# Performance work log

Hardware: AMD Instinct MI355X
Metric: run time of the kernel (lower is better)

Reference implementation:

```python
import jax, jax.numpy as jnp
import numpy as np

B, S, L = 2048, 1024, 32
NEG = -10000.0


def setup_inputs() -> dict:
    key = jax.random.key(0)
    k1, k2, k3, k4 = jax.random.split(key, 4)
    lstm_scores = jax.random.normal(k1, (B, S, L), dtype=jnp.float32)
    word_seq_lens = jax.random.randint(k2, (B,), 1, S + 1)  # lengths in [1, S]
    tags = jax.random.randint(k3, (B, S), 0, L - 3)  # real labels only
    mask = (jnp.arange(S)[None, :] < word_seq_lens[:, None])
    start_idx, end_idx, pad_idx = L - 1, L - 2, L - 3
    transition = jax.random.normal(k4, (L, L), dtype=jnp.float32)
    transition = (transition.at[:, start_idx].set(NEG)
                  .at[end_idx, :].set(NEG)
                  .at[:, pad_idx].set(NEG)
                  .at[pad_idx, :].set(NEG))
    return {"lstm_scores": lstm_scores, "transition": transition,
            "word_seq_lens": word_seq_lens, "tags": tags, "mask": mask}


def _crf_scores(lstm_scores, transition, word_seq_lens, tags, mask):
    b, s, l = lstm_scores.shape
    start_idx, end_idx = l - 1, l - 2

    # ---- forward algorithm (log partition) ----
    # all_scores[b,t,i,j] = transition[i,j] + lstm_scores[b,t,j]; fused into the scan step.
    alpha0 = transition[start_idx][None, :] + lstm_scores[:, 0, :]  # (B,L)

    def step(alpha_prev, emit_t):  # emit_t: (B,L)
        a = jax.nn.logsumexp(alpha_prev[:, :, None] + transition[None, :, :]
                             + emit_t[:, None, :], axis=1)  # (B,L)
        return a, a

    emits = jnp.swapaxes(lstm_scores, 0, 1)  # (S,B,L)
    _, alphas_rest = jax.lax.scan(step, alpha0, emits[1:])
    alphas = jnp.concatenate([alpha0[None], alphas_rest], axis=0)  # (S,B,L)

    last_alpha = alphas[word_seq_lens - 1, jnp.arange(b), :]  # (B,L)
    last_alpha = last_alpha + transition[:, end_idx][None, :]
    unlabeled = jnp.sum(jax.nn.logsumexp(last_alpha, axis=1))

    # ---- gold path score ----
    emit_at_tag = jnp.take_along_axis(lstm_scores, tags[:, :, None], axis=2)[..., 0]  # (B,S)
    begin = transition[start_idx, tags[:, 0]] + emit_at_tag[:, 0]  # (B,)
    trans_mid = transition[tags[:, :-1], tags[:, 1:]]  # (B,S-1)
    middle = trans_mid + emit_at_tag[:, 1:]  # (B,S-1)
    middle = jnp.where(mask[:, 1:], middle, 0.0)
    end_tags = tags[jnp.arange(b), word_seq_lens - 1]  # (B,)
    end = transition[end_tags, end_idx]  # (B,)
    labeled = jnp.sum(begin) + jnp.sum(middle) + jnp.sum(end)

    return unlabeled, labeled


def reference(lstm_scores, transition, word_seq_lens, tags, mask):
    return _crf_scores(lstm_scores, transition, word_seq_lens, tags, mask)
```

## Files before the change

### kernel.cpp

```cpp
#include <hip/hip_runtime.h>

#define NB 2048
#define NS 1024
#define NL 32

static __device__ __forceinline__ float fexp2(float x) {
#if __has_builtin(__builtin_amdgcn_exp2f)
  return __builtin_amdgcn_exp2f(x);
#else
  float r; asm("v_exp_f32 %0, %1" : "=v"(r) : "v"(x)); return r;
#endif
}
static __device__ __forceinline__ float flog2(float x) {
#if __has_builtin(__builtin_amdgcn_logf)
  return __builtin_amdgcn_logf(x);
#else
  float r; asm("v_log_f32 %0, %1" : "=v"(r) : "v"(x)); return r;
#endif
}

template<int K>
static __device__ __forceinline__ int roti(int x) {
  if constexpr (K == 0) return x;
  else return __builtin_amdgcn_update_dpp(0, x, 0x120 | K, 0xf, 0xf, true);
}

static __device__ __forceinline__ float plswap16_sum(float part) {
  float x, y;
  asm volatile("v_mov_b32 %0, %2\n\t"
               "v_mov_b32 %1, %2\n\t"
               "s_nop 1\n\t"
               "v_permlane16_swap_b32 %0, %1\n\t"
               "s_nop 1"
               : "=&v"(x), "=&v"(y) : "v"(part));
  return x + y;
}
static __device__ __forceinline__ float plswap32_sum(float part) {
  float x, y;
  asm volatile("v_mov_b32 %0, %2\n\t"
               "v_mov_b32 %1, %2\n\t"
               "s_nop 1\n\t"
               "v_permlane32_swap_b32 %0, %1\n\t"
               "s_nop 1"
               : "=&v"(x), "=&v"(y) : "v"(part));
  return x + y;
}
static __device__ __forceinline__ int plswap16_partner(int lane) {
  int x, y;
  asm volatile("v_mov_b32 %0, %2\n\t"
               "v_mov_b32 %1, %2\n\t"
               "s_nop 1\n\t"
               "v_permlane16_swap_b32 %0, %1\n\t"
               "s_nop 1"
               : "=&v"(x), "=&v"(y) : "v"(lane));
  return x + y - lane;
}

static __device__ __forceinline__ float tree16f(float p, const float* E) {
  float a0 = 0.0f, a1 = 0.0f, a2 = 0.0f, a3 = 0.0f;
  asm volatile(
    "s_nop 1\n\t"
    "v_mul_f32 %0, %4, %5\n\t"
    "v_mul_f32_dpp %1, %4, %6 row_ror:1 row_mask:0xf bank_mask:0xf\n\t"
    "v_mul_f32_dpp %2, %4, %7 row_ror:2 row_mask:0xf bank_mask:0xf\n\t"
    "v_mul_f32_dpp %3, %4, %8 row_ror:3 row_mask:0xf bank_mask:0xf\n\t"
    "v_fmac_f32_dpp %0, %4, %9 row_ror:4 row_mask:0xf bank_mask:0xf\n\t"
    "v_fmac_f32_dpp %1, %4, %10 row_ror:5 row_mask:0xf bank_mask:0xf\n\t"
    "v_fmac_f32_dpp %2, %4, %11 row_ror:6 row_mask:0xf bank_mask:0xf\n\t"
    "v_fmac_f32_dpp %3, %4, %12 row_ror:7 row_mask:0xf bank_mask:0xf\n\t"
    "v_fmac_f32_dpp %0, %4, %13 row_ror:8 row_mask:0xf bank_mask:0xf\n\t"
    "v_fmac_f32_dpp %1, %4, %14 row_ror:9 row_mask:0xf bank_mask:0xf\n\t"
    "v_fmac_f32_dpp %2, %4, %15 row_ror:10 row_mask:0xf bank_mask:0xf\n\t"
    "v_fmac_f32_dpp %3, %4, %16 row_ror:11 row_mask:0xf bank_mask:0xf\n\t"
    "v_fmac_f32_dpp %0, %4, %17 row_ror:12 row_mask:0xf bank_mask:0xf\n\t"
    "v_fmac_f32_dpp %1, %4, %18 row_ror:13 row_mask:0xf bank_mask:0xf\n\t"
    "v_fmac_f32_dpp %2, %4, %19 row_ror:14 row_mask:0xf bank_mask:0xf\n\t"
    "v_fmac_f32_dpp %3, %4, %20 row_ror:15 row_mask:0xf bank_mask:0xf"
    : "+v"(a0), "+v"(a1), "+v"(a2), "+v"(a3)
    : "v"(p),
      "v"(E[0]),  "v"(E[1]),  "v"(E[2]),  "v"(E[3]),
      "v"(E[4]),  "v"(E[5]),  "v"(E[6]),  "v"(E[7]),
      "v"(E[8]),  "v"(E[9]),  "v"(E[10]), "v"(E[11]),
      "v"(E[12]), "v"(E[13]), "v"(E[14]), "v"(E[15]));
  return (a0 + a1) + (a2 + a3);
}

__global__ void zero_out_k(float* out) {
  if (threadIdx.x < 2) out[threadIdx.x] = 0.0f;
}

__global__ __launch_bounds__(1024)
void sort_perm_k(const int* __restrict__ lens, int* __restrict__ perm) {
  __shared__ int h0[1024], h1[1024];
  const int tid = threadIdx.x;
  h0[tid] = 0;
  __syncthreads();
  for (int i = tid; i < NB; i += 1024) atomicAdd(&h0[1024 - lens[i]], 1);
  __syncthreads();
  const int cnt = h0[tid];
  int* src = h0; int* dst = h1;
  for (int off = 1; off < 1024; off <<= 1) {
    dst[tid] = src[tid] + ((tid >= off) ? src[tid - off] : 0);
    __syncthreads();
    int* tmp = src; src = dst; dst = tmp;
  }
  const int excl = src[tid] - cnt;
  __syncthreads();
  dst[tid] = excl;
  __syncthreads();
  for (int i = tid; i < NB; i += 1024) {
    const int key = 1024 - lens[i];
    const int pos = atomicAdd(&dst[key], 1);
    perm[pos] = i;
  }
}

__global__ __launch_bounds__(128, 2)
void crf_fwd(const float* __restrict__ scores, const float* __restrict__ trans,
             const int* __restrict__ lens, const int* __restrict__ tags,
             const int* __restrict__ perm, float* __restrict__ out)
{
  constexpr float LOG2E = 1.4426950408889634f;
  constexpr float LN2   = 0.6931471805599453f;
  __shared__ float Tld[NL * NL];
  __shared__ float slotm[64];

  const int b    = perm ? perm[blockIdx.x] : blockIdx.x;
  const int tid  = threadIdx.x;
  const int wid  = tid >> 6;
  const int lane = tid & 63;
  const int len  = lens[b];
  const int m    = len >> 1;
  const int nB   = len - 1 - m;
  const int r = lane >> 4, c = lane & 15;
  const int labA = c + ((r & 1) << 4);

  const int p16 = plswap16_partner(lane);
  const bool plOK = ((p16 & 15) == c) && ((((p16 >> 4) ^ r) & 1) == 1);
  const int pmax = (lane > p16) ? lane : p16;
  const int labB = plOK ? (c + ((pmax >= 48) ? 16 : 0))
                        : (c + (((r >> 1) & 1) << 4));

  const float* sbf = scores + (size_t)b * (NS * NL);

  for (int k2 = tid; k2 < NL * NL; k2 += 128) Tld[k2] = trans[k2] * LOG2E;
  __syncthreads();

#define COMB16(S) (plOK ? plswap16_sum(S) : ((S) + __shfl_xor((S), 16)))
#define LDROW(DST, ROW, LAB) do { \
    int r_ = (ROW); r_ = r_ < 0 ? 0 : r_; r_ = r_ > len - 1 ? len - 1 : r_; \
    DST = sbf[(size_t)r_ * NL + (LAB)]; \
  } while (0)

  float u, ls;
  bool endB = false;

  if (wid == 0) {
    float EA[16], EB[16];
#define CFA(K) EA[K] = fexp2(Tld[roti<K>(labA) * NL + labB]);
#define CFB(K) EB[K] = fexp2(Tld[roti<K>(labB) * NL + labA]);
    CFA(0)  CFA(1)  CFA(2)  CFA(3)  CFA(4)  CFA(5)  CFA(6)  CFA(7)
    CFA(8)  CFA(9)  CFA(10) CFA(11) CFA(12) CFA(13) CFA(14) CFA(15)
    CFB(0)  CFB(1)  CFB(2)  CFB(3)  CFB(4)  CFB(5)  CFB(6)  CFB(7)
    CFB(8)  CFB(9)  CFB(10) CFB(11) CFB(12) CFB(13) CFB(14) CFB(15)
#undef CFA
#undef CFB
    float a0 = Tld[31 * NL + labA] + LOG2E * sbf[labA];
    ls = __int_as_float(__builtin_amdgcn_readfirstlane(__float_as_int(a0)));
    u = fexp2(a0 - ls);

#define RENORM do { \
    const int eb_ = __builtin_amdgcn_readfirstlane(__float_as_int(u)); \
    const int ex_ = (eb_ >> 23) - 127; \
    ls += (float)ex_; \
    u *= __int_as_float((127 - ex_) << 23); \
  } while (0)

    float P0, P1, P2, P3, Q0, Q1, Q2, Q3;
    int t = 1;
    LDROW(P0, 1, labB); LDROW(P1, 2, labA); LDROW(P2, 3, labB); LDROW(P3, 4, labA);
    LDROW(Q0, 5, labB); LDROW(Q1, 6, labA); LDROW(Q2, 7, labB); LDROW(Q3, 8, labA);

#define FBODY(B0, B1, B2, B3) do { \
    RENORM; \
    const float w0 = fexp2(B0 * LOG2E); \
    const float w1 = fexp2(B1 * LOG2E); \
    const float w2 = fexp2(B2 * LOG2E); \
    const float w3 = fexp2(B3 * LOG2E); \
    LDROW(B0, t + 8,  labB); LDROW(B1, t + 9,  labA); \
    LDROW(B2, t + 10, labB); LDROW(B3, t + 11, labA); \
    u = COMB16(tree16f(u, EA)) * w0; \
    u = plswap32_sum(tree16f(u, EB)) * w1; \
    u = COMB16(tree16f(u, EA)) * w2; \
    u = plswap32_sum(tree16f(u, EB)) * w3; \
  } while (0)

    while (t + 7 <= m) {
      FBODY(P0, P1, P2, P3); t += 4;
      FBODY(Q0, Q1, Q2, Q3); t += 4;
    }
    if (t + 3 <= m) { FBODY(P0, P1, P2, P3); t += 4; }
    while (t <= m) {
      if ((t & 3) == 1) RENORM;
      if (t & 1) {
        float e; LDROW(e, t, labB);
        u = COMB16(tree16f(u, EA)) * fexp2(e * LOG2E);
        endB = true;
      } else {
        float e; LDROW(e, t, labA);
        u = plswap32_sum(tree16f(u, EB)) * fexp2(e * LOG2E);
        endB = false;
      }
      t++;
    }
#undef FBODY
  } else {
    float EA[16], EB[16];
#define CBA(K) EA[K] = fexp2(Tld[labB * NL + roti<K>(labA)]);
#define CBB(K) EB[K] = fexp2(Tld[labA * NL + roti<K>(labB)]);
    CBA(0)  CBA(1)  CBA(2)  CBA(3)  CBA(4)  CBA(5)  CBA(6)  CBA(7)
    CBA(8)  CBA(9)  CBA(10) CBA(11) CBA(12) CBA(13) CBA(14) CBA(15)
    CBB(0)  CBB(1)  CBB(2)  CBB(3)  CBB(4)  CBB(5)  CBB(6)  CBB(7)
    CBB(8)  CBB(9)  CBB(10) CBB(11) CBB(12) CBB(13) CBB(14) CBB(15)
#undef CBA
#undef CBB
    float a0 = Tld[labA * NL + 30];
    ls = __int_as_float(__builtin_amdgcn_readfirstlane(__float_as_int(a0)));
    u = fexp2(a0 - ls);

#define RENORMB do { \
    const int eb_ = __builtin_amdgcn_readfirstlane(__float_as_int(u)); \
    const int ex_ = (eb_ >> 23) - 127; \
    ls += (float)ex_; \
    u *= __int_as_float((127 - ex_) << 23); \
  } while (0)

    float P0, P1, P2, P3, Q0, Q1, Q2, Q3;
    int k = 0;
    LDROW(P0, len - 1, labA); LDROW(P1, len - 2, labB);
    LDROW(P2, len - 3, labA); LDROW(P3, len - 4, labB);
    LDROW(Q0, len - 5, labA); LDROW(Q1, len - 6, labB);
    LDROW(Q2, len - 7, labA); LDROW(Q3, len - 8, labB);

#define BBODY(B0, B1, B2, B3) do { \
    RENORMB; \
    const float w0 = fexp2(B0 * LOG2E); \
    const float w1 = fexp2(B1 * LOG2E); \
    const float w2 = fexp2(B2 * LOG2E); \
    const float w3 = fexp2(B3 * LOG2E); \
    LDROW(B0, len - 1 - k - 8,  labA); LDROW(B1, len - 2 - k - 8,  labB); \
    LDROW(B2, len - 3 - k - 8,  labA); LDROW(B3, len - 4 - k - 8,  labB); \
    u = COMB16(tree16f(u * w0, EA)); \
    u = plswap32_sum(tree16f(u * w1, EB)); \
    u = COMB16(tree16f(u * w2, EA)); \
    u = plswap32_sum(tree16f(u * w3, EB)); \
  } while (0)

    while (k + 7 < nB) {
      BBODY(P0, P1, P2, P3); k += 4;
      BBODY(Q0, Q1, Q2, Q3); k += 4;
    }
    if (k + 3 < nB) { BBODY(P0, P1, P2, P3); k += 4; }
    while (k < nB) {
      if ((k & 3) == 0) RENORMB;
      if (!(k & 1)) {
        float e; LDROW(e, len - 1 - k, labA);
        u = COMB16(tree16f(u * fexp2(e * LOG2E), EA));
        endB = true;
      } else {
        float e; LDROW(e, len - 1 - k, labB);
        u = plswap32_sum(tree16f(u * fexp2(e * LOG2E), EB));
        endB = false;
      }
      k++;
    }
#undef BBODY
#undef RENORMB
  }

  slotm[wid * 32 + (endB ? labB : labA)] = ls + flog2(u);
  __syncthreads();

  if (wid == 0) {
    float v2 = (lane < 32) ? (slotm[lane] + slotm[32 + lane]) : -3.0e38f;
    float mm = v2;
    #pragma unroll
    for (int w = 32; w; w >>= 1) mm = fmaxf(mm, __shfl_xor(mm, w));
    float ssum = fexp2(v2 - mm);
    #pragma unroll
    for (int w = 32; w; w >>= 1) ssum += __shfl_xor(ssum, w);
    if (lane == 0) atomicAdd(out + 0, LN2 * (mm + flog2(ssum)));

    const int* tb = tags + (size_t)b * NS;
    float lab = 0.0f;
    if (lane == 0) {
      const int tg0 = tb[0];
      lab += Tld[31 * NL + tg0] + LOG2E * sbf[tg0];
      const int tgl = tb[len - 1];
      lab += Tld[tgl * NL + 30];
    }
    for (int t2 = 1 + lane; t2 < len; t2 += 64) {
      const int tp = tb[t2 - 1];
      const int tg = tb[t2];
      lab += Tld[tp * NL + tg] + LOG2E * sbf[(size_t)t2 * NL + tg];
    }
    #pragma unroll
    for (int w = 32; w; w >>= 1) lab += __shfl_xor(lab, w);
    if (lane == 0) atomicAdd(out + 1, LN2 * lab);
  }
#undef COMB16
#undef LDROW
#undef RENORM
}

extern "C" void kernel_launch(void* const* d_in, const int* in_sizes, int n_in,
                              void* d_out, int out_size, void* d_ws, size_t ws_size,
                              hipStream_t stream) {
  const float* scores = (const float*)d_in[0];
  const float* trans  = (const float*)d_in[1];
  const int*   lens   = (const int*)d_in[2];
  const int*   tags   = (const int*)d_in[3];
  float* out = (float*)d_out;

  int* perm = (ws_size >= NB * sizeof(int)) ? (int*)d_ws : nullptr;

  zero_out_k<<<1, 64, 0, stream>>>(out);
  if (perm) sort_perm_k<<<1, 1024, 0, stream>>>(lens, perm);
  crf_fwd<<<NB, 128, 0, stream>>>(scores, trans, lens, tags, perm, out);
}
```

Before: 120.8 us.

## Split CRF scan into four segments with MFMA transfer-matrix products for middle chunks

Each sequence's forward recursion is now split across four waves. Wave 0 runs the forward pass over the first chunk and wave 3 runs the backward pass over the last. Waves 1 and 2 build 32x32 transfer-matrix products for the two middle chunks with bf16 MFMA, renormalising each step. Wave 0 then applies both matrices to stitch the result together, which shortens the serial dependency chain per block, and the gold-path sum moves to wave 1. In exchange there is bf16 precision loss in the middle matrices, heavier per-step work (a 32x32 matmul instead of a vector step), and 256-thread blocks with a higher occupancy bound.

```diff
diff --git a/kernel.cpp b/kernel.cpp
--- a/kernel.cpp
+++ b/kernel.cpp
@@ -3,6 +3,10 @@
 #define NB 2048
 #define NS 1024
 #define NL 32
+
+typedef short bf16x8 __attribute__((ext_vector_type(8)));
+typedef float f32x16 __attribute__((ext_vector_type(16)));
+union FragU { unsigned u[4]; bf16x8 v; };
 
 static __device__ __forceinline__ float fexp2(float x) {
 #if __has_builtin(__builtin_amdgcn_exp2f)
@@ -25,35 +29,46 @@
   else return __builtin_amdgcn_update_dpp(0, x, 0x120 | K, 0xf, 0xf, true);
 }
 
+static __device__ __forceinline__ void plswap32_pair(unsigned &x, unsigned &y) {
+  asm volatile("s_nop 1\n\tv_permlane32_swap_b32 %0, %1\n\ts_nop 1"
+               : "+v"(x), "+v"(y));
+}
 static __device__ __forceinline__ float plswap16_sum(float part) {
   float x, y;
-  asm volatile("v_mov_b32 %0, %2\n\t"
-               "v_mov_b32 %1, %2\n\t"
-               "s_nop 1\n\t"
-               "v_permlane16_swap_b32 %0, %1\n\t"
-               "s_nop 1"
+  asm volatile("v_mov_b32 %0, %2\n\tv_mov_b32 %1, %2\n\ts_nop 1\n\t"
+               "v_permlane16_swap_b32 %0, %1\n\ts_nop 1"
                : "=&v"(x), "=&v"(y) : "v"(part));
   return x + y;
 }
 static __device__ __forceinline__ float plswap32_sum(float part) {
   float x, y;
-  asm volatile("v_mov_b32 %0, %2\n\t"
-               "v_mov_b32 %1, %2\n\t"
-               "s_nop 1\n\t"
-               "v_permlane32_swap_b32 %0, %1\n\t"
-               "s_nop 1"
+  asm volatile("v_mov_b32 %0, %2\n\tv_mov_b32 %1, %2\n\ts_nop 1\n\t"
+               "v_permlane32_swap_b32 %0, %1\n\ts_nop 1"
                : "=&v"(x), "=&v"(y) : "v"(part));
   return x + y;
 }
+static __device__ __forceinline__ float plswap32_max(float part) {
+  float x, y;
+  asm volatile("v_mov_b32 %0, %2\n\tv_mov_b32 %1, %2\n\ts_nop 1\n\t"
+               "v_permlane32_swap_b32 %0, %1\n\ts_nop 1"
+               : "=&v"(x), "=&v"(y) : "v"(part));
+  return fmaxf(x, y);
+}
 static __device__ __forceinline__ int plswap16_partner(int lane) {
   int x, y;
-  asm volatile("v_mov_b32 %0, %2\n\t"
-               "v_mov_b32 %1, %2\n\t"
-               "s_nop 1\n\t"
-               "v_permlane16_swap_b32 %0, %1\n\t"
-               "s_nop 1"
+  asm volatile("v_mov_b32 %0, %2\n\tv_mov_b32 %1, %2\n\ts_nop 1\n\t"
+               "v_permlane16_swap_b32 %0, %1\n\ts_nop 1"
                : "=&v"(x), "=&v"(y) : "v"(lane));
   return x + y - lane;
+}
+
+static __device__ __forceinline__ unsigned cvtpk(float a, float b) {
+  unsigned r;
+  asm("v_cvt_pk_bf16_f32 %0, %1, %2" : "=v"(r) : "v"(a), "v"(b));
+  return r;
+}
+static __device__ __forceinline__ float bf2f(unsigned short u) {
+  return __int_as_float(((int)u) << 16);
 }
 
 static __device__ __forceinline__ float tree16f(float p, const float* E) {
@@ -115,7 +130,7 @@
   }
 }
 
-__global__ __launch_bounds__(128, 2)
+__global__ __launch_bounds__(256, 4)
 void crf_fwd(const float* __restrict__ scores, const float* __restrict__ trans,
              const int* __restrict__ lens, const int* __restrict__ tags,
              const int* __restrict__ perm, float* __restrict__ out)
@@ -123,17 +138,25 @@
   constexpr float LOG2E = 1.4426950408889634f;
   constexpr float LN2   = 0.6931471805599453f;
   __shared__ float Tld[NL * NL];
+  __shared__ alignas(16) unsigned short Mb[2][NL * NL];
+  __shared__ float Xls[2][NL];
   __shared__ float slotm[64];
 
   const int b    = perm ? perm[blockIdx.x] : blockIdx.x;
   const int tid  = threadIdx.x;
-  const int wid  = tid >> 6;
+  const int w    = tid >> 6;
   const int lane = tid & 63;
   const int len  = lens[b];
-  const int m    = len >> 1;
-  const int nB   = len - 1 - m;
+  const int nsteps = len - 1;
+  const int Lm = (3 * nsteps) / 19;
+  const int c1 = (nsteps - 2 * Lm + 1) >> 1;
+  const int c2 = c1 + Lm;
+  const int c3 = c2 + Lm;
+  const int nBw = nsteps - c3;
   const int r = lane >> 4, c = lane & 15;
   const int labA = c + ((r & 1) << 4);
+  const int col  = lane & 31;
+  const int half = lane >> 5;
 
   const int p16 = plswap16_partner(lane);
   const bool plOK = ((p16 & 15) == c) && ((((p16 >> 4) ^ r) & 1) == 1);
@@ -141,9 +164,13 @@
   const int labB = plOK ? (c + ((pmax >= 48) ? 16 : 0))
                         : (c + (((r >> 1) & 1) << 4));
 
+  unsigned px = half ? 200u : 100u, py = half ? 400u : 300u;
+  plswap32_pair(px, py);
+  const bool dirC1 = (__builtin_amdgcn_readfirstlane(px) == 100u);
+
   const float* sbf = scores + (size_t)b * (NS * NL);
 
-  for (int k2 = tid; k2 < NL * NL; k2 += 128) Tld[k2] = trans[k2] * LOG2E;
+  for (int k2 = tid; k2 < NL * NL; k2 += 256) Tld[k2] = trans[k2] * LOG2E;
   __syncthreads();
 
 #define COMB16(S) (plOK ? plswap16_sum(S) : ((S) + __shfl_xor((S), 16)))
@@ -151,11 +178,17 @@
     int r_ = (ROW); r_ = r_ < 0 ? 0 : r_; r_ = r_ > len - 1 ? len - 1 : r_; \
     DST = sbf[(size_t)r_ * NL + (LAB)]; \
   } while (0)
-
-  float u, ls;
+#define RENU do { \
+    const int eb_ = __builtin_amdgcn_readfirstlane(__float_as_int(u)); \
+    const int ex_ = (eb_ >> 23) - 127; \
+    ls += (float)ex_; \
+    u *= __int_as_float((127 - ex_) << 23); \
+  } while (0)
+
+  float u = 1.0f, ls = 0.0f;
   bool endB = false;
 
-  if (wid == 0) {
+  if (w == 0) {
     float EA[16], EB[16];
 #define CFA(K) EA[K] = fexp2(Tld[roti<K>(labA) * NL + labB]);
 #define CFB(K) EB[K] = fexp2(Tld[roti<K>(labB) * NL + labA]);
@@ -169,20 +202,13 @@
     ls = __int_as_float(__builtin_amdgcn_readfirstlane(__float_as_int(a0)));
     u = fexp2(a0 - ls);
 
-#define RENORM do { \
-    const int eb_ = __builtin_amdgcn_readfirstlane(__float_as_int(u)); \
-    const int ex_ = (eb_ >> 23) - 127; \
-    ls += (float)ex_; \
-    u *= __int_as_float((127 - ex_) << 23); \
-  } while (0)
-
     float P0, P1, P2, P3, Q0, Q1, Q2, Q3;
     int t = 1;
     LDROW(P0, 1, labB); LDROW(P1, 2, labA); LDROW(P2, 3, labB); LDROW(P3, 4, labA);
     LDROW(Q0, 5, labB); LDROW(Q1, 6, labA); LDROW(Q2, 7, labB); LDROW(Q3, 8, labA);
 
 #define FBODY(B0, B1, B2, B3) do { \
-    RENORM; \
+    RENU; \
     const float w0 = fexp2(B0 * LOG2E); \
     const float w1 = fexp2(B1 * LOG2E); \
     const float w2 = fexp2(B2 * LOG2E); \
@@ -195,13 +221,13 @@
     u = plswap32_sum(tree16f(u, EB)) * w3; \
   } while (0)
 
-    while (t + 7 <= m) {
+    while (t + 7 <= c1) {
       FBODY(P0, P1, P2, P3); t += 4;
       FBODY(Q0, Q1, Q2, Q3); t += 4;
     }
-    if (t + 3 <= m) { FBODY(P0, P1, P2, P3); t += 4; }
-    while (t <= m) {
-      if ((t & 3) == 1) RENORM;
+    if (t + 3 <= c1) { FBODY(P0, P1, P2, P3); t += 4; }
+    while (t <= c1) {
+      if ((t & 3) == 1) RENU;
       if (t & 1) {
         float e; LDROW(e, t, labB);
         u = COMB16(tree16f(u, EA)) * fexp2(e * LOG2E);
@@ -214,7 +240,7 @@
       t++;
     }
 #undef FBODY
-  } else {
+  } else if (w == 3) {
     float EA[16], EB[16];
 #define CBA(K) EA[K] = fexp2(Tld[labB * NL + roti<K>(labA)]);
 #define CBB(K) EB[K] = fexp2(Tld[labA * NL + roti<K>(labB)]);
@@ -228,13 +254,6 @@
     ls = __int_as_float(__builtin_amdgcn_readfirstlane(__float_as_int(a0)));
     u = fexp2(a0 - ls);
 
-#define RENORMB do { \
-    const int eb_ = __builtin_amdgcn_readfirstlane(__float_as_int(u)); \
-    const int ex_ = (eb_ >> 23) - 127; \
-    ls += (float)ex_; \
-    u *= __int_as_float((127 - ex_) << 23); \
-  } while (0)
-
     float P0, P1, P2, P3, Q0, Q1, Q2, Q3;
     int k = 0;
     LDROW(P0, len - 1, labA); LDROW(P1, len - 2, labB);
@@ -243,7 +262,7 @@
     LDROW(Q2, len - 7, labA); LDROW(Q3, len - 8, labB);
 
 #define BBODY(B0, B1, B2, B3) do { \
-    RENORMB; \
+    RENU; \
     const float w0 = fexp2(B0 * LOG2E); \
     const float w1 = fexp2(B1 * LOG2E); \
     const float w2 = fexp2(B2 * LOG2E); \
@@ -256,13 +275,13 @@
     u = plswap32_sum(tree16f(u * w3, EB)); \
   } while (0)
 
-    while (k + 7 < nB) {
+    while (k + 7 < nBw) {
       BBODY(P0, P1, P2, P3); k += 4;
       BBODY(Q0, Q1, Q2, Q3); k += 4;
     }
-    if (k + 3 < nB) { BBODY(P0, P1, P2, P3); k += 4; }
-    while (k < nB) {
-      if ((k & 3) == 0) RENORMB;
+    if (k + 3 < nBw) { BBODY(P0, P1, P2, P3); k += 4; }
+    while (k < nBw) {
+      if ((k & 3) == 0) RENU;
       if (!(k & 1)) {
         float e; LDROW(e, len - 1 - k, labA);
         u = COMB16(tree16f(u * fexp2(e * LOG2E), EA));
@@ -275,22 +294,146 @@
       k++;
     }
 #undef BBODY
-#undef RENORMB
+    slotm[32 + (endB ? labB : labA)] = ls + flog2(u);
+  } else {
+    const int mi = w - 1;
+    const int t0 = (w == 1 ? c1 + 1 : c2 + 1);
+    const int v  = Lm;
+
+    if (v == 0) {
+      unsigned* mw = (unsigned*)&Mb[mi][0];
+      #pragma unroll
+      for (int q = 0; q < 8; ++q) mw[lane + 64 * q] = 0u;
+      asm volatile("s_waitcnt lgkmcnt(0)" ::: "memory");
+      if (lane < 32) { Mb[mi][lane * NL + lane] = 0x3F80; Xls[mi][lane] = 0.0f; }
+    } else {
+      float EAb1[8], EAb2[8];
+      #pragma unroll
+      for (int p = 0; p < 8; ++p) {
+        EAb1[p] = fexp2(Tld[(8 * half + p) * NL + col]);
+        EAb2[p] = fexp2(Tld[(16 + 8 * half + p) * NL + col]);
+      }
+      f32x16 acc;
+      #pragma unroll
+      for (int i = 0; i < 16; ++i) {
+        const int row = (i & 3) + 8 * (i >> 2) + 4 * half;
+        acc[i] = (row == col) ? 1.0f : 0.0f;
+      }
+      float Xw = 0.0f;
+
+#define MLDW(T) sbf[(size_t)(((T) > len - 1) ? (len - 1) : (T)) * NL + col]
+      float er0 = MLDW(t0 + 0), er1 = MLDW(t0 + 1), er2 = MLDW(t0 + 2), er3 = MLDW(t0 + 3);
+      float er4 = MLDW(t0 + 4), er5 = MLDW(t0 + 5), er6 = MLDW(t0 + 6), er7 = MLDW(t0 + 7);
+
+#define MSTEP(EQ) do { \
+    const float ws_ = fexp2((EQ) * LOG2E); \
+    FragU a1_, a2_, b1_, b2_; \
+    _Pragma("unroll") \
+    for (int p_ = 0; p_ < 4; ++p_) { \
+      a1_.u[p_] = cvtpk(EAb1[2 * p_] * ws_, EAb1[2 * p_ + 1] * ws_); \
+      a2_.u[p_] = cvtpk(EAb2[2 * p_] * ws_, EAb2[2 * p_ + 1] * ws_); \
+    } \
+    unsigned pk0_ = cvtpk(acc[0],  acc[1]),  pk1_ = cvtpk(acc[2],  acc[3]); \
+    unsigned pk2_ = cvtpk(acc[4],  acc[5]),  pk3_ = cvtpk(acc[6],  acc[7]); \
+    unsigned pk4_ = cvtpk(acc[8],  acc[9]),  pk5_ = cvtpk(acc[10], acc[11]); \
+    unsigned pk6_ = cvtpk(acc[12], acc[13]), pk7_ = cvtpk(acc[14], acc[15]); \
+    if (dirC1) { \
+      plswap32_pair(pk0_, pk2_); b1_.u[0] = pk0_; b1_.u[2] = pk2_; \
+      plswap32_pair(pk1_, pk3_); b1_.u[1] = pk1_; b1_.u[3] = pk3_; \
+      plswap32_pair(pk4_, pk6_); b2_.u[0] = pk4_; b2_.u[2] = pk6_; \
+      plswap32_pair(pk5_, pk7_); b2_.u[1] = pk5_; b2_.u[3] = pk7_; \
+    } else { \
+      plswap32_pair(pk2_, pk0_); b1_.u[2] = pk2_; b1_.u[0] = pk0_; \
+      plswap32_pair(pk3_, pk1_); b1_.u[3] = pk3_; b1_.u[1] = pk1_; \
+      plswap32_pair(pk6_, pk4_); b2_.u[2] = pk6_; b2_.u[0] = pk4_; \
+      plswap32_pair(pk7_, pk5_); b2_.u[3] = pk7_; b2_.u[1] = pk5_; \
+    } \
+    f32x16 z_; \
+    _Pragma("unroll") \
+    for (int i_ = 0; i_ < 16; ++i_) z_[i_] = 0.0f; \
+    z_  = __builtin_amdgcn_mfma_f32_32x32x16_bf16(a1_.v, b1_.v, z_, 0, 0, 0); \
+    acc = __builtin_amdgcn_mfma_f32_32x32x16_bf16(a2_.v, b2_.v, z_, 0, 0, 0); \
+    float mx_ = fmaxf(fmaxf(fmaxf(acc[0], acc[1]), fmaxf(acc[2], acc[3])), \
+                      fmaxf(fmaxf(acc[4], acc[5]), fmaxf(acc[6], acc[7]))); \
+    mx_ = fmaxf(mx_, fmaxf(fmaxf(fmaxf(acc[8], acc[9]), fmaxf(acc[10], acc[11])), \
+                           fmaxf(fmaxf(acc[12], acc[13]), fmaxf(acc[14], acc[15])))); \
+    mx_ = plswap32_max(mx_); \
+    const int ex_ = (__float_as_int(mx_) >> 23) - 127; \
+    const float rs_ = __int_as_float((127 - ex_) << 23); \
+    _Pragma("unroll") \
+    for (int i_ = 0; i_ < 16; ++i_) acc[i_] *= rs_; \
+    Xw += (float)ex_; \
+  } while (0)
+
+      int sg = 0;
+      while (sg + 8 <= v) {
+        MSTEP(er0); er0 = MLDW(t0 + sg + 8);
+        MSTEP(er1); er1 = MLDW(t0 + sg + 9);
+        MSTEP(er2); er2 = MLDW(t0 + sg + 10);
+        MSTEP(er3); er3 = MLDW(t0 + sg + 11);
+        MSTEP(er4); er4 = MLDW(t0 + sg + 12);
+        MSTEP(er5); er5 = MLDW(t0 + sg + 13);
+        MSTEP(er6); er6 = MLDW(t0 + sg + 14);
+        MSTEP(er7); er7 = MLDW(t0 + sg + 15);
+        sg += 8;
+      }
+      if (sg + 0 < v) MSTEP(er0);
+      if (sg + 1 < v) MSTEP(er1);
+      if (sg + 2 < v) MSTEP(er2);
+      if (sg + 3 < v) MSTEP(er3);
+      if (sg + 4 < v) MSTEP(er4);
+      if (sg + 5 < v) MSTEP(er5);
+      if (sg + 6 < v) MSTEP(er6);
+      if (sg + 7 < v) MSTEP(er7);
+
+      {
+        unsigned* mw32 = (unsigned*)&Mb[mi][0];
+        #pragma unroll
+        for (int j = 0; j < 8; ++j) {
+          const int row0 = (2 * j & 3) + 8 * (2 * j >> 2) + 4 * half;
+          mw32[(col * NL + row0) >> 1] = cvtpk(acc[2 * j], acc[2 * j + 1]);
+        }
+      }
+      if (lane < 32) Xls[mi][col] = Xw;
+#undef MSTEP
+#undef MLDW
+    }
   }
 
-  slotm[wid * 32 + (endB ? labB : labA)] = ls + flog2(u);
-  __syncthreads();
-
-  if (wid == 0) {
+  __syncthreads();
+
+  if (w == 0) {
+    bool curB = endB;
+    for (int cdx = 0; cdx < 2; ++cdx) {
+      const int held = curB ? labB : labA;
+      const int outl = curB ? labA : labB;
+      const float dX = Xls[cdx][held];
+      const float X0 = __int_as_float(__builtin_amdgcn_readfirstlane(__float_as_int(dX)));
+      u *= fexp2(fminf(dX - X0, 120.0f));
+      ls += X0;
+      RENU;
+      float Ec[16];
+#define LDE(K) Ec[K] = bf2f(Mb[cdx][roti<K>(held) * NL + outl]);
+      LDE(0)  LDE(1)  LDE(2)  LDE(3)  LDE(4)  LDE(5)  LDE(6)  LDE(7)
+      LDE(8)  LDE(9)  LDE(10) LDE(11) LDE(12) LDE(13) LDE(14) LDE(15)
+#undef LDE
+      const float s16 = tree16f(u, Ec);
+      u = (!curB) ? COMB16(s16) : plswap32_sum(s16);
+      RENU;
+      curB = !curB;
+    }
+    slotm[curB ? labB : labA] = ls + flog2(u);
+    asm volatile("s_waitcnt lgkmcnt(0)" ::: "memory");
+
     float v2 = (lane < 32) ? (slotm[lane] + slotm[32 + lane]) : -3.0e38f;
     float mm = v2;
     #pragma unroll
-    for (int w = 32; w; w >>= 1) mm = fmaxf(mm, __shfl_xor(mm, w));
+    for (int ww = 32; ww; ww >>= 1) mm = fmaxf(mm, __shfl_xor(mm, ww));
     float ssum = fexp2(v2 - mm);
     #pragma unroll
-    for (int w = 32; w; w >>= 1) ssum += __shfl_xor(ssum, w);
+    for (int ww = 32; ww; ww >>= 1) ssum += __shfl_xor(ssum, ww);
     if (lane == 0) atomicAdd(out + 0, LN2 * (mm + flog2(ssum)));
-
+  } else if (w == 1) {
     const int* tb = tags + (size_t)b * NS;
     float lab = 0.0f;
     if (lane == 0) {
@@ -305,12 +448,12 @@
       lab += Tld[tp * NL + tg] + LOG2E * sbf[(size_t)t2 * NL + tg];
     }
     #pragma unroll
-    for (int w = 32; w; w >>= 1) lab += __shfl_xor(lab, w);
+    for (int ww = 32; ww; ww >>= 1) lab += __shfl_xor(lab, ww);
     if (lane == 0) atomicAdd(out + 1, LN2 * lab);
   }
 #undef COMB16
 #undef LDROW
-#undef RENORM
+#undef RENU
 }
 
 extern "C" void kernel_launch(void* const* d_in, const int* in_sizes, int n_in,
@@ -326,5 +469,5 @@
 
   zero_out_k<<<1, 64, 0, stream>>>(out);
   if (perm) sort_perm_k<<<1, 1024, 0, stream>>>(lens, perm);
-  crf_fwd<<<NB, 128, 0, stream>>>(scores, trans, lens, tags, perm, out);
-}
+  crf_fwd<<<NB, 256, 0, stream>>>(scores, trans, lens, tags, perm, out);
+}
```

Result: slower. 132.2 us (+9.4%).
